# Kernel tuning notes

Hardware: AMD Instinct MI355X
Metric: run time of the kernel (lower is better)

The kernel has to match this reference:

```python
import jax, jax.numpy as jnp
import numpy as np

IN_FEATURES = 256
OUT_FEATURES = 512
NUM_SEGMENTS = 8
GRID_MIN, GRID_MAX = -1.0, 1.0
STEP = (GRID_MAX - GRID_MIN) / NUM_SEGMENTS
LN_EPS = 1e-5


def setup_inputs() -> dict:
    key = jax.random.key(0)
    k1, k2 = jax.random.split(key)
    B = 2048
    x = jax.random.normal(k1, (B, IN_FEATURES), dtype=jnp.float32)
    # Xavier-uniform a_embed, zeros b_embed, as in reset_parameters
    vocab = IN_FEATURES * NUM_SEGMENTS
    limit = float(np.sqrt(6.0 / (vocab + OUT_FEATURES)))
    a_weight = jax.random.uniform(k2, (vocab, OUT_FEATURES), minval=-limit, maxval=limit, dtype=jnp.float32)
    b_weight = jnp.zeros((vocab, OUT_FEATURES), dtype=jnp.float32)
    gamma = jnp.ones((IN_FEATURES,), dtype=jnp.float32)
    beta = jnp.zeros((IN_FEATURES,), dtype=jnp.float32)
    return {"x": x, "a_weight": a_weight, "b_weight": b_weight, "gamma": gamma, "beta": beta}


def reference(x, a_weight, b_weight, gamma, beta):
    # LayerNorm over in_features
    mu = jnp.mean(x, axis=-1, keepdims=True)
    var = jnp.mean(jnp.square(x - mu), axis=-1, keepdims=True)
    xn = (x - mu) * jax.lax.rsqrt(var + LN_EPS) * gamma + beta  # [B, I]

    # data-dependent segment index (torch .long() truncates; clamp makes trunc==floor here)
    float_idx = (xn - GRID_MIN) / STEP
    seg = jnp.clip(float_idx.astype(jnp.int32), 0, NUM_SEGMENTS - 1)  # [B, I]
    global_idx = seg + jnp.arange(IN_FEATURES, dtype=jnp.int32)[None, :] * NUM_SEGMENTS

    a_vals = a_weight[global_idx]  # [B, I, O]
    b_vals = b_weight[global_idx]  # [B, I, O]
    # sum over in_features of a*x + b
    y = jnp.einsum('bi,bio->bo', xn, a_vals) + jnp.sum(b_vals, axis=1)
    return y
```

## Files before the change

### kernel.cpp

```cpp
#include <hip/hip_runtime.h>

#define I_FEAT 256
#define O_FEAT 512
#define NSEG   8
#define KDIM   (I_FEAT * NSEG)
#define KTOT   (2 * KDIM)
#define KC_N   (KTOT / 32)

typedef _Float16 half8   __attribute__((ext_vector_type(8)));
typedef float    floatx4 __attribute__((ext_vector_type(4)));
typedef uint32_t uintx4  __attribute__((ext_vector_type(4)));

__global__ __launch_bounds__(256) void prep(
    const float* __restrict__ x,
    const float* __restrict__ Aw,
    const float* __restrict__ Bw,
    const float* __restrict__ gamma,
    const float* __restrict__ beta,
    uint4* __restrict__ Bf,
    uint2* __restrict__ Am,
    int Bn, int pbTot)
{
    __shared__ char smem[16 * 260 * 4];
    const int t   = threadIdx.x;
    const int bid = blockIdx.x;

    if (bid < pbTot) {
        unsigned short (*T)[72] = (unsigned short(*)[72])smem;
        const int n0 = (bid & 7) * 64;
        const int k0 = (bid >> 3) * 64;
        const float* src = (k0 < KDIM) ? (Aw + (size_t)k0 * O_FEAT)
                                       : (Bw + (size_t)(k0 - KDIM) * O_FEAT);
        #pragma unroll
        for (int s = 0; s < 4; ++s) {
            int e  = s * 1024 + t * 4;
            int kl = e >> 6, nl = e & 63;
            const float4 v = *(const float4*)(src + (size_t)kl * O_FEAT + n0 + nl);
            T[nl + 0][kl] = __builtin_bit_cast(unsigned short, (_Float16)v.x);
            T[nl + 1][kl] = __builtin_bit_cast(unsigned short, (_Float16)v.y);
            T[nl + 2][kl] = __builtin_bit_cast(unsigned short, (_Float16)v.z);
            T[nl + 3][kl] = __builtin_bit_cast(unsigned short, (_Float16)v.w);
        }
        __syncthreads();

        const int lane = t & 63, lane16 = lane & 15, quad = lane >> 4;
        const int sub  = t >> 6;
        #pragma unroll
        for (int f = 0; f < 2; ++f) {
            const int combo = sub * 2 + f;
            const int n16g  = combo & 3;
            const int kch   = combo >> 2;
            const int nl = n16g * 16 + lane16;
            const int kl = kch * 32 + quad * 8;
            const uint4 val = *(const uint4*)&T[nl][kl];
            const int n16t = (n0 >> 4) + n16g;
            const int kc   = (k0 >> 5) + kch;
            Bf[((size_t)n16t * KC_N + kc) * 64 + lane] = val;
        }
    } else {
        uint32_t (*M)[260] = (uint32_t(*)[260])smem;
        const int mt16 = bid - pbTot;
        const int rr   = t >> 4;
        const int c16  = t & 15;
        const int row  = mt16 * 16 + rr;
        const bool ok  = (row < Bn);

        float4 v[4];
        const float* xr = x + (size_t)row * I_FEAT + c16 * 16;
        #pragma unroll
        for (int j = 0; j < 4; ++j)
            v[j] = ok ? *(const float4*)(xr + j * 4) : make_float4(0.f, 0.f, 0.f, 0.f);

        float sum = 0.f, sq = 0.f;
        #pragma unroll
        for (int j = 0; j < 4; ++j) {
            sum += v[j].x + v[j].y + v[j].z + v[j].w;
            sq  += v[j].x * v[j].x + v[j].y * v[j].y
                 + v[j].z * v[j].z + v[j].w * v[j].w;
        }
        #pragma unroll
        for (int mask = 1; mask < 16; mask <<= 1) {
            sum += __shfl_xor(sum, mask);
            sq  += __shfl_xor(sq,  mask);
        }
        const float mu  = sum * (1.0f / I_FEAT);
        const float var = sq * (1.0f / I_FEAT) - mu * mu;
        const float rs  = rsqrtf(var + 1e-5f);

        #pragma unroll
        for (int j = 0; j < 4; ++j) {
            const float4 g4 = *(const float4*)(gamma + c16 * 16 + j * 4);
            const float4 b4 = *(const float4*)(beta  + c16 * 16 + j * 4);
            const float vv[4] = { v[j].x, v[j].y, v[j].z, v[j].w };
            const float gg[4] = { g4.x, g4.y, g4.z, g4.w };
            const float bb[4] = { b4.x, b4.y, b4.z, b4.w };
            #pragma unroll
            for (int e = 0; e < 4; ++e) {
                const int c = c16 * 16 + j * 4 + e;
                float xn = (vv[e] - mu) * rs * gg[e] + bb[e];
                float fi = (xn + 1.0f) * 4.0f;
                int seg = (int)fi;
                seg = seg < 0 ? 0 : (seg > NSEG - 1 ? NSEG - 1 : seg);
                _Float16 hx = (_Float16)xn;
                M[rr][c] = ((uint32_t)seg << 16)
                         | (uint32_t)__builtin_bit_cast(unsigned short, hx);
            }
        }
        __syncthreads();

        const int lane = t & 63, g = t >> 6;
        const int m_local = lane & 15, quad = lane >> 4;
        uint2* dst = Am + (size_t)mt16 * 64 * 64 + lane;
        #pragma unroll
        for (int kk = 0; kk < 16; ++kk) {
            const int kcp = g * 16 + kk;
            const int w0  = kcp * 8 + quad;
            const int w1  = w0 + 4;
            const uint32_t u0 = M[m_local][w0 & 255];
            const uint32_t u1 = M[m_local][w1 & 255];
            const uint32_t a  = (w0 >> 8) ? ((u0 & 0xFFFF0000u) | 0x3C00u) : u0;
            const uint32_t b  = (w1 >> 8) ? ((u1 & 0xFFFF0000u) | 0x3C00u) : u1;
            dst[(size_t)kcp * 64] = make_uint2(a, b);
        }
    }
}

static __device__ __forceinline__ half8 build_onehot(uint32_t u) {
    const uint32_t xb  = u & 0xFFFFu;
    const uint32_t seg = u >> 16;
    const uint64_t oh  = (uint64_t)xb << ((seg & 3u) << 4);
    const uint64_t lo  = (seg < 4u) ? oh : 0ull;
    const uint64_t hi  = (seg < 4u) ? 0ull : oh;
    uintx4 w;
    w[0] = (uint32_t)lo; w[1] = (uint32_t)(lo >> 32);
    w[2] = (uint32_t)hi; w[3] = (uint32_t)(hi >> 32);
    return __builtin_bit_cast(half8, w);
}

__global__ __launch_bounds__(256, 2) void kan_gemm(
    const uint2* __restrict__ Am,
    const uint4* __restrict__ Bf,
    float* __restrict__ out,
    int Bn, int rt64Tot)
{
    __shared__ floatx4 s_red[4][8][64];

    const int t      = threadIdx.x;
    const int wave   = t >> 6, lane = t & 63;
    const int lane16 = lane & 15, quad = lane >> 4;
    const int bid    = blockIdx.x;

    int ot, rt;
    if (rt64Tot == 32) {
        const int xc = bid & 7, j = bid >> 3;
        ot = ((j >> 4) << 2) | (xc & 3);
        rt = (j & 15) | ((xc >> 2) << 4);
    } else {
        ot = bid & 15;
        rt = bid >> 4;
    }

    const uint2* pa = Am + (size_t)(rt * 4) * 64 * 64 + lane;
    const uint4* pb = Bf + (size_t)(ot * 2) * KC_N * 64 + lane;

    floatx4 acc[4][2] = {};
    const int kcp0 = wave * 16;

    #pragma unroll 4
    for (int p = 0; p < 16; ++p) {
        const int kcp = kcp0 + p;
        const uint2 u0 = pa[(size_t)kcp * 64];
        const uint2 u1 = pa[(size_t)(4096  + kcp * 64)];
        const uint2 u2 = pa[(size_t)(8192  + kcp * 64)];
        const uint2 u3 = pa[(size_t)(12288 + kcp * 64)];
        const uint4 b00 = pb[(size_t)(2 * kcp + 0) * 64];
        const uint4 b01 = pb[(size_t)(2 * kcp + 1) * 64];
        const uint4 b10 = pb[(size_t)(8192 + (2 * kcp + 0) * 64)];
        const uint4 b11 = pb[(size_t)(8192 + (2 * kcp + 1) * 64)];
        {
            const half8 n0 = __builtin_bit_cast(half8, b00);
            const half8 n1 = __builtin_bit_cast(half8, b10);
            half8 a;
            a = build_onehot(u0.x);
            acc[0][0] = __builtin_amdgcn_mfma_f32_16x16x32_f16(a, n0, acc[0][0], 0, 0, 0);
            acc[0][1] = __builtin_amdgcn_mfma_f32_16x16x32_f16(a, n1, acc[0][1], 0, 0, 0);
            a = build_onehot(u1.x);
            acc[1][0] = __builtin_amdgcn_mfma_f32_16x16x32_f16(a, n0, acc[1][0], 0, 0, 0);
            acc[1][1] = __builtin_amdgcn_mfma_f32_16x16x32_f16(a, n1, acc[1][1], 0, 0, 0);
            a = build_onehot(u2.x);
            acc[2][0] = __builtin_amdgcn_mfma_f32_16x16x32_f16(a, n0, acc[2][0], 0, 0, 0);
            acc[2][1] = __builtin_amdgcn_mfma_f32_16x16x32_f16(a, n1, acc[2][1], 0, 0, 0);
            a = build_onehot(u3.x);
            acc[3][0] = __builtin_amdgcn_mfma_f32_16x16x32_f16(a, n0, acc[3][0], 0, 0, 0);
            acc[3][1] = __builtin_amdgcn_mfma_f32_16x16x32_f16(a, n1, acc[3][1], 0, 0, 0);
        }
        {
            const half8 n0 = __builtin_bit_cast(half8, b01);
            const half8 n1 = __builtin_bit_cast(half8, b11);
            half8 a;
            a = build_onehot(u0.y);
            acc[0][0] = __builtin_amdgcn_mfma_f32_16x16x32_f16(a, n0, acc[0][0], 0, 0, 0);
            acc[0][1] = __builtin_amdgcn_mfma_f32_16x16x32_f16(a, n1, acc[0][1], 0, 0, 0);
            a = build_onehot(u1.y);
            acc[1][0] = __builtin_amdgcn_mfma_f32_16x16x32_f16(a, n0, acc[1][0], 0, 0, 0);
            acc[1][1] = __builtin_amdgcn_mfma_f32_16x16x32_f16(a, n1, acc[1][1], 0, 0, 0);
            a = build_onehot(u2.y);
            acc[2][0] = __builtin_amdgcn_mfma_f32_16x16x32_f16(a, n0, acc[2][0], 0, 0, 0);
            acc[2][1] = __builtin_amdgcn_mfma_f32_16x16x32_f16(a, n1, acc[2][1], 0, 0, 0);
            a = build_onehot(u3.y);
            acc[3][0] = __builtin_amdgcn_mfma_f32_16x16x32_f16(a, n0, acc[3][0], 0, 0, 0);
            acc[3][1] = __builtin_amdgcn_mfma_f32_16x16x32_f16(a, n1, acc[3][1], 0, 0, 0);
        }
    }

    #pragma unroll
    for (int mi = 0; mi < 4; ++mi)
        #pragma unroll
        for (int ni = 0; ni < 2; ++ni)
            s_red[wave][mi * 2 + ni][lane] = acc[mi][ni];
    __syncthreads();

    #pragma unroll
    for (int q = 0; q < 2; ++q) {
        const int tt = wave * 2 + q;
        const int mi = tt >> 1, ni = tt & 1;
        floatx4 vsum = s_red[0][tt][lane];
        vsum += s_red[1][tt][lane];
        vsum += s_red[2][tt][lane];
        vsum += s_red[3][tt][lane];
        const int gcol = ot * 32 + ni * 16 + lane16;
        const int gr0  = rt * 64 + mi * 16 + quad * 4;
        #pragma unroll
        for (int r = 0; r < 4; ++r) {
            const int grow = gr0 + r;
            if (grow < Bn)
                out[(size_t)grow * O_FEAT + gcol] = vsum[r];
        }
    }
}

extern "C" void kernel_launch(void* const* d_in, const int* in_sizes, int n_in,
                              void* d_out, int out_size, void* d_ws, size_t ws_size,
                              hipStream_t stream) {
    const float* x   = (const float*)d_in[0];
    const float* Aw  = (const float*)d_in[1];
    const float* Bw  = (const float*)d_in[2];
    const float* gam = (const float*)d_in[3];
    const float* bet = (const float*)d_in[4];
    float* out       = (float*)d_out;

    const int Bn      = in_sizes[0] / I_FEAT;
    const int mt16Tot = (Bn + 15) / 16;
    const int rt64Tot = (Bn + 63) / 64;
    const int pbTot   = (O_FEAT / 64) * (KTOT / 64);

    uint4* Bf = (uint4*)d_ws;
    uint2* Am = (uint2*)(Bf + (size_t)(O_FEAT / 16) * KC_N * 64);

    hipLaunchKernelGGL(prep, dim3(pbTot + mt16Tot), dim3(256), 0, stream,
                       x, Aw, Bw, gam, bet, Bf, Am, Bn, pbTot);
    hipLaunchKernelGGL(kan_gemm, dim3(16 * rt64Tot), dim3(256), 0, stream,
                       Am, Bf, out, Bn, rt64Tot);
}
```

Baseline: 87.85 us.

## Pair A and B weight chunks per one-hot so activations halve and prep skips smem

The activation buffer now stores only the 256 real features (32 k-chunk pairs instead of 64) and no longer holds the padded 'ones' rows for the b_weight half. The GEMM builds two one-hot fragments from each packed word, one scaled by x and one by 1.0, and multiplies them against matching A and B weight chunks. The weight-prep path is rewritten to read strided fp32 columns directly and pack fp16 fragments without an LDS transpose. The intent is to halve activation loads and prep writes while keeping the MFMA count the same. The cost is uncoalesced column loads in prep and extra register pressure in the GEMM.

```diff
diff --git a/kernel.cpp b/kernel.cpp
--- a/kernel.cpp
+++ b/kernel.cpp
@@ -4,8 +4,8 @@
 #define O_FEAT 512
 #define NSEG   8
 #define KDIM   (I_FEAT * NSEG)
-#define KTOT   (2 * KDIM)
-#define KC_N   (KTOT / 32)
+#define KC_N   128
+#define KCP_A  32
 
 typedef _Float16 half8   __attribute__((ext_vector_type(8)));
 typedef float    floatx4 __attribute__((ext_vector_type(4)));
@@ -19,47 +19,39 @@
     const float* __restrict__ beta,
     uint4* __restrict__ Bf,
     uint2* __restrict__ Am,
-    int Bn, int pbTot)
+    int Bn, int pkTot)
 {
-    __shared__ char smem[16 * 260 * 4];
+    __shared__ uint32_t M[16][260];
     const int t   = threadIdx.x;
     const int bid = blockIdx.x;
-
-    if (bid < pbTot) {
-        unsigned short (*T)[72] = (unsigned short(*)[72])smem;
-        const int n0 = (bid & 7) * 64;
-        const int k0 = (bid >> 3) * 64;
-        const float* src = (k0 < KDIM) ? (Aw + (size_t)k0 * O_FEAT)
-                                       : (Bw + (size_t)(k0 - KDIM) * O_FEAT);
-        #pragma unroll
-        for (int s = 0; s < 4; ++s) {
-            int e  = s * 1024 + t * 4;
-            int kl = e >> 6, nl = e & 63;
-            const float4 v = *(const float4*)(src + (size_t)kl * O_FEAT + n0 + nl);
-            T[nl + 0][kl] = __builtin_bit_cast(unsigned short, (_Float16)v.x);
-            T[nl + 1][kl] = __builtin_bit_cast(unsigned short, (_Float16)v.y);
-            T[nl + 2][kl] = __builtin_bit_cast(unsigned short, (_Float16)v.z);
-            T[nl + 3][kl] = __builtin_bit_cast(unsigned short, (_Float16)v.w);
-        }
-        __syncthreads();
-
-        const int lane = t & 63, lane16 = lane & 15, quad = lane >> 4;
-        const int sub  = t >> 6;
-        #pragma unroll
-        for (int f = 0; f < 2; ++f) {
-            const int combo = sub * 2 + f;
-            const int n16g  = combo & 3;
-            const int kch   = combo >> 2;
-            const int nl = n16g * 16 + lane16;
-            const int kl = kch * 32 + quad * 8;
-            const uint4 val = *(const uint4*)&T[nl][kl];
-            const int n16t = (n0 >> 4) + n16g;
-            const int kc   = (k0 >> 5) + kch;
-            Bf[((size_t)n16t * KC_N + kc) * 64 + lane] = val;
+    const int lane = t & 63, lane16 = lane & 15, quad = lane >> 4;
+
+    if (bid < pkTot) {
+        const int ng   = bid & 7;
+        const int kg   = bid >> 3;
+        const int wave = t >> 6;
+        const int n16t = ng * 4 + wave;
+        const int n    = n16t * 16 + lane16;
+        #pragma unroll
+        for (int kk = 0; kk < 4; ++kk) {
+            const int kc = kg * 4 + kk;
+            const int k0 = kc * 32 + quad * 8;
+            const float* src = (kc < 64) ? (Aw + (size_t)k0 * O_FEAT + n)
+                                         : (Bw + (size_t)(k0 - KDIM) * O_FEAT + n);
+            float f[8];
+            #pragma unroll
+            for (int j = 0; j < 8; ++j) f[j] = src[(size_t)j * O_FEAT];
+            uintx4 w;
+            #pragma unroll
+            for (int jj = 0; jj < 4; ++jj) {
+                const uint32_t l0 = (uint32_t)__builtin_bit_cast(unsigned short, (_Float16)f[2 * jj]);
+                const uint32_t h0 = (uint32_t)__builtin_bit_cast(unsigned short, (_Float16)f[2 * jj + 1]);
+                w[jj] = (h0 << 16) | l0;
+            }
+            Bf[((size_t)n16t * KC_N + kc) * 64 + lane] = __builtin_bit_cast(uint4, w);
         }
     } else {
-        uint32_t (*M)[260] = (uint32_t(*)[260])smem;
-        const int mt16 = bid - pbTot;
+        const int mt16 = bid - pkTot;
         const int rr   = t >> 4;
         const int c16  = t & 15;
         const int row  = mt16 * 16 + rr;
@@ -108,34 +100,36 @@
         }
         __syncthreads();
 
-        const int lane = t & 63, g = t >> 6;
-        const int m_local = lane & 15, quad = lane >> 4;
-        uint2* dst = Am + (size_t)mt16 * 64 * 64 + lane;
-        #pragma unroll
-        for (int kk = 0; kk < 16; ++kk) {
-            const int kcp = g * 16 + kk;
+        const int g = t >> 6;
+        uint2* dst = Am + (size_t)mt16 * (KCP_A * 64) + lane;
+        #pragma unroll
+        for (int kk = 0; kk < 8; ++kk) {
+            const int kcp = g * 8 + kk;
             const int w0  = kcp * 8 + quad;
-            const int w1  = w0 + 4;
-            const uint32_t u0 = M[m_local][w0 & 255];
-            const uint32_t u1 = M[m_local][w1 & 255];
-            const uint32_t a  = (w0 >> 8) ? ((u0 & 0xFFFF0000u) | 0x3C00u) : u0;
-            const uint32_t b  = (w1 >> 8) ? ((u1 & 0xFFFF0000u) | 0x3C00u) : u1;
-            dst[(size_t)kcp * 64] = make_uint2(a, b);
-        }
-    }
-}
-
-static __device__ __forceinline__ half8 build_onehot(uint32_t u) {
+            dst[(size_t)kcp * 64] = make_uint2(M[lane16][w0], M[lane16][w0 + 4]);
+        }
+    }
+}
+
+static __device__ __forceinline__ void build_pair(uint32_t u, half8& ax, half8& a1) {
     const uint32_t xb  = u & 0xFFFFu;
     const uint32_t seg = u >> 16;
-    const uint64_t oh  = (uint64_t)xb << ((seg & 3u) << 4);
-    const uint64_t lo  = (seg < 4u) ? oh : 0ull;
-    const uint64_t hi  = (seg < 4u) ? 0ull : oh;
-    uintx4 w;
-    w[0] = (uint32_t)lo; w[1] = (uint32_t)(lo >> 32);
-    w[2] = (uint32_t)hi; w[3] = (uint32_t)(hi >> 32);
-    return __builtin_bit_cast(half8, w);
-}
+    const uint32_t sh  = (seg & 3u) << 4;
+    const uint64_t ox  = (uint64_t)xb << sh;
+    const uint64_t o1  = 0x3C00ull << sh;
+    const bool lo = (seg < 4u);
+    const uint32_t oxl = (uint32_t)ox, oxh = (uint32_t)(ox >> 32);
+    const uint32_t o1l = (uint32_t)o1, o1h = (uint32_t)(o1 >> 32);
+    uintx4 wx, w1;
+    wx[0] = lo ? oxl : 0u;  wx[1] = lo ? oxh : 0u;
+    wx[2] = lo ? 0u : oxl;  wx[3] = lo ? 0u : oxh;
+    w1[0] = lo ? o1l : 0u;  w1[1] = lo ? o1h : 0u;
+    w1[2] = lo ? 0u : o1l;  w1[3] = lo ? 0u : o1h;
+    ax = __builtin_bit_cast(half8, wx);
+    a1 = __builtin_bit_cast(half8, w1);
+}
+
+#define MFMA16 __builtin_amdgcn_mfma_f32_16x16x32_f16
 
 __global__ __launch_bounds__(256, 2) void kan_gemm(
     const uint2* __restrict__ Am,
@@ -160,57 +154,47 @@
         rt = bid >> 4;
     }
 
-    const uint2* pa = Am + (size_t)(rt * 4) * 64 * 64 + lane;
+    const uint2* pa = Am + (size_t)(rt * 4) * (KCP_A * 64) + lane;
     const uint4* pb = Bf + (size_t)(ot * 2) * KC_N * 64 + lane;
 
     floatx4 acc[4][2] = {};
-    const int kcp0 = wave * 16;
-
-    #pragma unroll 4
-    for (int p = 0; p < 16; ++p) {
+    const int kcp0 = wave * 8;
+
+    #pragma unroll 2
+    for (int p = 0; p < 8; ++p) {
         const int kcp = kcp0 + p;
-        const uint2 u0 = pa[(size_t)kcp * 64];
-        const uint2 u1 = pa[(size_t)(4096  + kcp * 64)];
-        const uint2 u2 = pa[(size_t)(8192  + kcp * 64)];
-        const uint2 u3 = pa[(size_t)(12288 + kcp * 64)];
-        const uint4 b00 = pb[(size_t)(2 * kcp + 0) * 64];
-        const uint4 b01 = pb[(size_t)(2 * kcp + 1) * 64];
-        const uint4 b10 = pb[(size_t)(8192 + (2 * kcp + 0) * 64)];
-        const uint4 b11 = pb[(size_t)(8192 + (2 * kcp + 1) * 64)];
-        {
-            const half8 n0 = __builtin_bit_cast(half8, b00);
-            const half8 n1 = __builtin_bit_cast(half8, b10);
-            half8 a;
-            a = build_onehot(u0.x);
-            acc[0][0] = __builtin_amdgcn_mfma_f32_16x16x32_f16(a, n0, acc[0][0], 0, 0, 0);
-            acc[0][1] = __builtin_amdgcn_mfma_f32_16x16x32_f16(a, n1, acc[0][1], 0, 0, 0);
-            a = build_onehot(u1.x);
-            acc[1][0] = __builtin_amdgcn_mfma_f32_16x16x32_f16(a, n0, acc[1][0], 0, 0, 0);
-            acc[1][1] = __builtin_amdgcn_mfma_f32_16x16x32_f16(a, n1, acc[1][1], 0, 0, 0);
-            a = build_onehot(u2.x);
-            acc[2][0] = __builtin_amdgcn_mfma_f32_16x16x32_f16(a, n0, acc[2][0], 0, 0, 0);
-            acc[2][1] = __builtin_amdgcn_mfma_f32_16x16x32_f16(a, n1, acc[2][1], 0, 0, 0);
-            a = build_onehot(u3.x);
-            acc[3][0] = __builtin_amdgcn_mfma_f32_16x16x32_f16(a, n0, acc[3][0], 0, 0, 0);
-            acc[3][1] = __builtin_amdgcn_mfma_f32_16x16x32_f16(a, n1, acc[3][1], 0, 0, 0);
-        }
-        {
-            const half8 n0 = __builtin_bit_cast(half8, b01);
-            const half8 n1 = __builtin_bit_cast(half8, b11);
-            half8 a;
-            a = build_onehot(u0.y);
-            acc[0][0] = __builtin_amdgcn_mfma_f32_16x16x32_f16(a, n0, acc[0][0], 0, 0, 0);
-            acc[0][1] = __builtin_amdgcn_mfma_f32_16x16x32_f16(a, n1, acc[0][1], 0, 0, 0);
-            a = build_onehot(u1.y);
-            acc[1][0] = __builtin_amdgcn_mfma_f32_16x16x32_f16(a, n0, acc[1][0], 0, 0, 0);
-            acc[1][1] = __builtin_amdgcn_mfma_f32_16x16x32_f16(a, n1, acc[1][1], 0, 0, 0);
-            a = build_onehot(u2.y);
-            acc[2][0] = __builtin_amdgcn_mfma_f32_16x16x32_f16(a, n0, acc[2][0], 0, 0, 0);
-            acc[2][1] = __builtin_amdgcn_mfma_f32_16x16x32_f16(a, n1, acc[2][1], 0, 0, 0);
-            a = build_onehot(u3.y);
-            acc[3][0] = __builtin_amdgcn_mfma_f32_16x16x32_f16(a, n0, acc[3][0], 0, 0, 0);
-            acc[3][1] = __builtin_amdgcn_mfma_f32_16x16x32_f16(a, n1, acc[3][1], 0, 0, 0);
-        }
+        const uint2 u0 = pa[(size_t)(kcp * 64)];
+        const uint2 u1 = pa[(size_t)(2048 + kcp * 64)];
+        const uint2 u2 = pa[(size_t)(4096 + kcp * 64)];
+        const uint2 u3 = pa[(size_t)(6144 + kcp * 64)];
+        const int kb = 2 * kcp;
+        const half8 e0  = __builtin_bit_cast(half8, pb[(size_t)((kb)      * 64)]);
+        const half8 q0  = __builtin_bit_cast(half8, pb[(size_t)((kb + 1)  * 64)]);
+        const half8 be0 = __builtin_bit_cast(half8, pb[(size_t)((kb + 64) * 64)]);
+        const half8 bq0 = __builtin_bit_cast(half8, pb[(size_t)((kb + 65) * 64)]);
+        const half8 e1  = __builtin_bit_cast(half8, pb[(size_t)(8192 + (kb)      * 64)]);
+        const half8 q1  = __builtin_bit_cast(half8, pb[(size_t)(8192 + (kb + 1)  * 64)]);
+        const half8 be1 = __builtin_bit_cast(half8, pb[(size_t)(8192 + (kb + 64) * 64)]);
+        const half8 bq1 = __builtin_bit_cast(half8, pb[(size_t)(8192 + (kb + 65) * 64)]);
+
+        half8 ax, av;
+#define ROWOP(r, uu) \
+        build_pair(uu.x, ax, av); \
+        acc[r][0] = MFMA16(ax, e0,  acc[r][0], 0, 0, 0); \
+        acc[r][1] = MFMA16(ax, e1,  acc[r][1], 0, 0, 0); \
+        acc[r][0] = MFMA16(av, be0, acc[r][0], 0, 0, 0); \
+        acc[r][1] = MFMA16(av, be1, acc[r][1], 0, 0, 0); \
+        build_pair(uu.y, ax, av); \
+        acc[r][0] = MFMA16(ax, q0,  acc[r][0], 0, 0, 0); \
+        acc[r][1] = MFMA16(ax, q1,  acc[r][1], 0, 0, 0); \
+        acc[r][0] = MFMA16(av, bq0, acc[r][0], 0, 0, 0); \
+        acc[r][1] = MFMA16(av, bq1, acc[r][1], 0, 0, 0);
+
+        ROWOP(0, u0)
+        ROWOP(1, u1)
+        ROWOP(2, u2)
+        ROWOP(3, u3)
+#undef ROWOP
     }
 
     #pragma unroll
@@ -252,13 +236,13 @@
     const int Bn      = in_sizes[0] / I_FEAT;
     const int mt16Tot = (Bn + 15) / 16;
     const int rt64Tot = (Bn + 63) / 64;
-    const int pbTot   = (O_FEAT / 64) * (KTOT / 64);
+    const int pkTot   = 256;
 
     uint4* Bf = (uint4*)d_ws;
     uint2* Am = (uint2*)(Bf + (size_t)(O_FEAT / 16) * KC_N * 64);
 
-    hipLaunchKernelGGL(prep, dim3(pbTot + mt16Tot), dim3(256), 0, stream,
-                       x, Aw, Bw, gam, bet, Bf, Am, Bn, pbTot);
+    hipLaunchKernelGGL(prep, dim3(pkTot + mt16Tot), dim3(256), 0, stream,
+                       x, Aw, Bw, gam, bet, Bf, Am, Bn, pkTot);
     hipLaunchKernelGGL(kan_gemm, dim3(16 * rt64Tot), dim3(256), 0, stream,
                        Am, Bf, out, Bn, rt64Tot);
 }
```

Result: no change. 88.45 us (+0.7%).
